# Optimization experiments

Hardware: AMD Instinct MI355X
Metric: run time of the kernel (lower is better)

## Reference

```python
import jax, jax.numpy as jnp
import numpy as np
from jax import lax

# Module constants (from init_kwargs)
K = 1.0            # conductivity
H = 1.0 / 1023.0   # grid spacing
VALUE = 0.0        # Dirichlet boundary value
STENCIL = np.array([[0.0, 0.25, 0.0],
                    [0.25, 0.0, 0.25],
                    [0.0, 0.25, 0.0]], dtype=np.float32)


def setup_inputs() -> dict:
    key = jax.random.key(0)
    k1, k2 = jax.random.split(key)
    B, C, Hn, Wn = 16, 1, 1024, 1024
    u = jax.random.normal(k1, (B, C, Hn, Wn), dtype=jnp.float32)
    f = jax.random.normal(k2, (B, C, Hn, Wn), dtype=jnp.float32)
    # conv weight: (out=1, in=1, 3, 3), repeated over in_channels (=1 here)
    weight = jnp.asarray(STENCIL).reshape(1, 1, 3, 3)
    return {"u": u, "f": f, "weight": weight}


def reference(u, f, weight):
    # v = detached interior of u, padded with the Dirichlet value
    v_int = lax.stop_gradient(u[..., 1:-1, 1:-1])           # [B,1,H-2,W-2]
    v = jnp.pad(v_int, ((0, 0), (0, 0), (1, 1), (1, 1)),
                mode="constant", constant_values=VALUE)      # [B,1,H,W]
    # 5-point Jacobi stencil, VALID conv -> interior shape [B,1,H-2,W-2]
    conv = lax.conv_general_dilated(
        v, weight, window_strides=(1, 1), padding="VALID",
        dimension_numbers=("NCHW", "OIHW", "NCHW"))
    cof = -(H ** 2) / (K * 4.0)
    source = lax.stop_gradient((cof * f)[..., 1:-1, 1:-1])
    # interior <- stencil(v) + source; boundary stays at Dirichlet VALUE
    out = v.at[..., 1:-1, 1:-1].set(conv + source)
    return out
```

## Files before the change

### kernel.cpp

```cpp
#include <hip/hip_runtime.h>

#define IMG_W 1024
#define IMG_H 1024
#define ROWS  8

typedef float v4f __attribute__((ext_vector_type(4)));

__global__ __launch_bounds__(256) void dir_rhs_kernel(
    const float* __restrict__ u,
    const float* __restrict__ f,
    const float* __restrict__ wt,
    float* __restrict__ out)
{
    const int tile = blockIdx.x;
    const int b    = tile >> 7;
    const int r0   = (tile & 127) << 3;
    const int tid  = threadIdx.x;
    const int j0   = tid << 2;
    const size_t img = (size_t)b << 20;

    const float* ub = u   + img;
    const float* fb = f   + img;
    float*       ob = out + img;

    const bool le = (j0 == 0);
    const bool re = (j0 + 4 >= IMG_W);

    const float w00 = wt[0], w01 = wt[1], w02 = wt[2];
    const float w10 = wt[3], w11 = wt[4], w12 = wt[5];
    const float w20 = wt[6], w21 = wt[7], w22 = wt[8];
    const float cof = (float)(-(1.0 / 1023.0) * (1.0 / 1023.0) / 4.0);

    float vm[6], vc[6], vp[6], nx[6];

    auto loadv = [&](float* a, int r) {
        if (r < 1 || r > IMG_H - 2) {
            #pragma unroll
            for (int q = 0; q < 6; q++) a[q] = 0.f;
            return;
        }
        const float* p = ub + (size_t)r * IMG_W;
        v4f c = *(const v4f*)(p + j0);
        a[1] = c.x; a[2] = c.y; a[3] = c.z; a[4] = c.w;
        a[0] = le ? 0.f : p[j0 - 1];
        a[5] = re ? 0.f : p[j0 + 4];
        if (le) a[1] = 0.f;
        if (re) a[4] = 0.f;
    };

    loadv(vm, r0 - 1);
    loadv(vc, r0);
    loadv(vp, r0 + 1);

    #pragma unroll
    for (int k = 0; k < ROWS; k++) {
        const int r = r0 + k;

        loadv(nx, r + 2);

        v4f* o4 = (v4f*)(ob + (size_t)r * IMG_W + j0);

        if (r == 0 || r == IMG_H - 1) {
            v4f z = {0.f, 0.f, 0.f, 0.f};
            __builtin_nontemporal_store(z, o4);
        } else {
            v4f f4 = *(const v4f*)(fb + (size_t)r * IMG_W + j0);
            float ff[4] = {f4.x, f4.y, f4.z, f4.w};

            float res[4];
            #pragma unroll
            for (int e = 0; e < 4; e++) {
                float acc = cof * ff[e];
                acc += w00 * vm[e] + w01 * vm[e + 1] + w02 * vm[e + 2];
                acc += w10 * vc[e] + w11 * vc[e + 1] + w12 * vc[e + 2];
                acc += w20 * vp[e] + w21 * vp[e + 1] + w22 * vp[e + 2];
                res[e] = acc;
            }
            if (le) res[0] = 0.f;
            if (re) res[3] = 0.f;

            v4f rv = {res[0], res[1], res[2], res[3]};
            __builtin_nontemporal_store(rv, o4);
        }

        #pragma unroll
        for (int q = 0; q < 6; q++) { vm[q] = vc[q]; vc[q] = vp[q]; vp[q] = nx[q]; }
    }
}

extern "C" void kernel_launch(void* const* d_in, const int* in_sizes, int n_in,
                              void* d_out, int out_size, void* d_ws, size_t ws_size,
                              hipStream_t stream) {
    const float* u  = (const float*)d_in[0];
    const float* f  = (const float*)d_in[1];
    const float* wt = (const float*)d_in[2];
    float* out = (float*)d_out;

    const int B = 16;
    dim3 grid(B * (IMG_H / ROWS));
    dim3 block(256);
    dir_rhs_kernel<<<grid, block, 0, stream>>>(u, f, wt, out);
}
```

Baseline: 174.4 us.

## Use wavefront shuffles for stencil halos, batch row loads, and swizzle block order

```diff
diff --git a/kernel.cpp b/kernel.cpp
--- a/kernel.cpp
+++ b/kernel.cpp
@@ -2,7 +2,7 @@
 
 #define IMG_W 1024
 #define IMG_H 1024
-#define ROWS  8
+#define ROWS  4
 
 typedef float v4f __attribute__((ext_vector_type(4)));
 
@@ -12,10 +12,13 @@
     const float* __restrict__ wt,
     float* __restrict__ out)
 {
-    const int tile = blockIdx.x;
-    const int b    = tile >> 7;
-    const int r0   = (tile & 127) << 3;
+    const int orig = blockIdx.x;
+    const int tile = (orig & 7) * 512 + (orig >> 3);
+
+    const int b    = tile >> 8;
+    const int r0   = (tile & 255) << 2;
     const int tid  = threadIdx.x;
+    const int lane = tid & 63;
     const int j0   = tid << 2;
     const size_t img = (size_t)b << 20;
 
@@ -24,67 +27,88 @@
     float*       ob = out + img;
 
     const bool le = (j0 == 0);
-    const bool re = (j0 + 4 >= IMG_W);
+    const bool re = (j0 == IMG_W - 4);
 
     const float w00 = wt[0], w01 = wt[1], w02 = wt[2];
     const float w10 = wt[3], w11 = wt[4], w12 = wt[5];
     const float w20 = wt[6], w21 = wt[7], w22 = wt[8];
     const float cof = (float)(-(1.0 / 1023.0) * (1.0 / 1023.0) / 4.0);
 
-    float vm[6], vc[6], vp[6], nx[6];
+    v4f ur[ROWS + 2];
+    #pragma unroll
+    for (int k = 0; k < ROWS + 2; k++) {
+        const int r = r0 - 1 + k;
+        const bool valid = (r >= 1) && (r <= IMG_H - 2);
+        if (valid) {
+            ur[k] = *(const v4f*)(ub + (size_t)r * IMG_W + j0);
+        } else {
+            ur[k] = (v4f){0.f, 0.f, 0.f, 0.f};
+        }
+    }
+    v4f fr[ROWS];
+    #pragma unroll
+    for (int k = 0; k < ROWS; k++) {
+        const int r = r0 + k;
+        if (r >= 1 && r <= IMG_H - 2) {
+            fr[k] = *(const v4f*)(fb + (size_t)r * IMG_W + j0);
+        } else {
+            fr[k] = (v4f){0.f, 0.f, 0.f, 0.f};
+        }
+    }
 
-    auto loadv = [&](float* a, int r) {
-        if (r < 1 || r > IMG_H - 2) {
-            #pragma unroll
-            for (int q = 0; q < 6; q++) a[q] = 0.f;
-            return;
-        }
-        const float* p = ub + (size_t)r * IMG_W;
-        v4f c = *(const v4f*)(p + j0);
-        a[1] = c.x; a[2] = c.y; a[3] = c.z; a[4] = c.w;
-        a[0] = le ? 0.f : p[j0 - 1];
-        a[5] = re ? 0.f : p[j0 + 4];
-        if (le) a[1] = 0.f;
-        if (re) a[4] = 0.f;
-    };
+    float lft[ROWS + 2], rgt[ROWS + 2];
+    #pragma unroll
+    for (int k = 0; k < ROWS + 2; k++) {
+        const int r = r0 - 1 + k;
+        const bool valid = (r >= 1) && (r <= IMG_H - 2);
+        float l  = __shfl_up(ur[k].w, 1);
+        float rr = __shfl_down(ur[k].x, 1);
+        if (valid && lane == 0  && !le) l  = ub[(size_t)r * IMG_W + j0 - 1];
+        if (valid && lane == 63 && !re) rr = ub[(size_t)r * IMG_W + j0 + 4];
+        lft[k] = (le || !valid) ? 0.f : l;
+        rgt[k] = (re || !valid) ? 0.f : rr;
+    }
 
-    loadv(vm, r0 - 1);
-    loadv(vc, r0);
-    loadv(vp, r0 + 1);
+    if (le) {
+        #pragma unroll
+        for (int k = 0; k < ROWS + 2; k++) ur[k].x = 0.f;
+    }
+    if (re) {
+        #pragma unroll
+        for (int k = 0; k < ROWS + 2; k++) ur[k].w = 0.f;
+    }
 
     #pragma unroll
     for (int k = 0; k < ROWS; k++) {
         const int r = r0 + k;
-
-        loadv(nx, r + 2);
-
         v4f* o4 = (v4f*)(ob + (size_t)r * IMG_W + j0);
 
         if (r == 0 || r == IMG_H - 1) {
             v4f z = {0.f, 0.f, 0.f, 0.f};
             __builtin_nontemporal_store(z, o4);
         } else {
-            v4f f4 = *(const v4f*)(fb + (size_t)r * IMG_W + j0);
-            float ff[4] = {f4.x, f4.y, f4.z, f4.w};
-
-            float res[4];
-            #pragma unroll
-            for (int e = 0; e < 4; e++) {
-                float acc = cof * ff[e];
-                acc += w00 * vm[e] + w01 * vm[e + 1] + w02 * vm[e + 2];
-                acc += w10 * vc[e] + w11 * vc[e + 1] + w12 * vc[e + 2];
-                acc += w20 * vp[e] + w21 * vp[e + 1] + w22 * vp[e + 2];
-                res[e] = acc;
-            }
-            if (le) res[0] = 0.f;
-            if (re) res[3] = 0.f;
-
-            v4f rv = {res[0], res[1], res[2], res[3]};
+            const v4f n = ur[k], c = ur[k + 1], s = ur[k + 2];
+            float res0 = cof * fr[k].x
+                       + w00 * lft[k]     + w01 * n.x + w02 * n.y
+                       + w10 * lft[k + 1] + w11 * c.x + w12 * c.y
+                       + w20 * lft[k + 2] + w21 * s.x + w22 * s.y;
+            float res1 = cof * fr[k].y
+                       + w00 * n.x + w01 * n.y + w02 * n.z
+                       + w10 * c.x + w11 * c.y + w12 * c.z
+                       + w20 * s.x + w21 * s.y + w22 * s.z;
+            float res2 = cof * fr[k].z
+                       + w00 * n.y + w01 * n.z + w02 * n.w
+                       + w10 * c.y + w11 * c.z + w12 * c.w
+                       + w20 * s.y + w21 * s.z + w22 * s.w;
+            float res3 = cof * fr[k].w
+                       + w00 * n.z + w01 * n.w + w02 * rgt[k]
+                       + w10 * c.z + w11 * c.w + w12 * rgt[k + 1]
+                       + w20 * s.z + w21 * s.w + w22 * rgt[k + 2];
+            if (le) res0 = 0.f;
+            if (re) res3 = 0.f;
+            v4f rv = {res0, res1, res2, res3};
             __builtin_nontemporal_store(rv, o4);
         }
-
-        #pragma unroll
-        for (int q = 0; q < 6; q++) { vm[q] = vc[q]; vc[q] = vp[q]; vp[q] = nx[q]; }
     }
 }
 
```

After: 180.2 us. +3.3%, slower.

## Process two rows per block with branchless masked loads and XCD-aware tile swizzle

Applied to the files above, without the earlier changes.

```diff
diff --git a/kernel.cpp b/kernel.cpp
--- a/kernel.cpp
+++ b/kernel.cpp
@@ -2,9 +2,9 @@
 
 #define IMG_W 1024
 #define IMG_H 1024
-#define ROWS  8
 
 typedef float v4f __attribute__((ext_vector_type(4)));
+typedef float v2f __attribute__((ext_vector_type(2)));
 
 __global__ __launch_bounds__(256) void dir_rhs_kernel(
     const float* __restrict__ u,
@@ -12,80 +12,86 @@
     const float* __restrict__ wt,
     float* __restrict__ out)
 {
-    const int tile = blockIdx.x;
-    const int b    = tile >> 7;
-    const int r0   = (tile & 127) << 3;
-    const int tid  = threadIdx.x;
-    const int j0   = tid << 2;
+    const int orig = blockIdx.x;
+    const int tile = (orig & 7) * 1024 + (orig >> 3);
+
+    const int b   = tile >> 9;
+    const int i0  = (tile & 511) << 1;
+    const int tid = threadIdx.x;
+    const int j0  = tid << 2;
     const size_t img = (size_t)b << 20;
 
-    const float* ub = u   + img;
-    const float* fb = f   + img;
-    float*       ob = out + img;
+    const float* ub = u + img;
 
     const bool le = (j0 == 0);
-    const bool re = (j0 + 4 >= IMG_W);
+    const bool re = (j0 == IMG_W - 4);
+
+    const int jl = le ? 0         : j0 - 2;
+    const int jr = re ? IMG_W - 2 : j0 + 4;
+
+    v4f c4[4]; v2f lv[4], rv[4]; float m[4];
+    #pragma unroll
+    for (int k = 0; k < 4; k++) {
+        const int li = i0 - 1 + k;
+        const int rc = li < 0 ? 0 : (li > IMG_H - 1 ? IMG_H - 1 : li);
+        const float* p = ub + (size_t)rc * IMG_W;
+        c4[k] = *(const v4f*)(p + j0);
+        lv[k] = *(const v2f*)(p + jl);
+        rv[k] = *(const v2f*)(p + jr);
+        m[k]  = (li >= 1 && li <= IMG_H - 2) ? 1.f : 0.f;
+    }
+    const float* fp = f + img + (size_t)i0 * IMG_W + j0;
+    const v4f f0 = __builtin_nontemporal_load((const v4f*)fp);
+    const v4f f1 = __builtin_nontemporal_load((const v4f*)(fp + IMG_W));
 
     const float w00 = wt[0], w01 = wt[1], w02 = wt[2];
     const float w10 = wt[3], w11 = wt[4], w12 = wt[5];
     const float w20 = wt[6], w21 = wt[7], w22 = wt[8];
     const float cof = (float)(-(1.0 / 1023.0) * (1.0 / 1023.0) / 4.0);
 
-    float vm[6], vc[6], vp[6], nx[6];
+    float lh[4], rh[4];
+    #pragma unroll
+    for (int k = 0; k < 4; k++) {
+        lh[k] = le ? 0.f : lv[k].y * m[k];
+        rh[k] = re ? 0.f : rv[k].x * m[k];
+        c4[k] = c4[k] * m[k];
+        if (le) c4[k].x = 0.f;
+        if (re) c4[k].w = 0.f;
+    }
 
-    auto loadv = [&](float* a, int r) {
-        if (r < 1 || r > IMG_H - 2) {
-            #pragma unroll
-            for (int q = 0; q < 6; q++) a[q] = 0.f;
-            return;
-        }
-        const float* p = ub + (size_t)r * IMG_W;
-        v4f c = *(const v4f*)(p + j0);
-        a[1] = c.x; a[2] = c.y; a[3] = c.z; a[4] = c.w;
-        a[0] = le ? 0.f : p[j0 - 1];
-        a[5] = re ? 0.f : p[j0 + 4];
-        if (le) a[1] = 0.f;
-        if (re) a[4] = 0.f;
+    const float keep0 = (i0 >= 1)         ? 1.f : 0.f;
+    const float keep1 = (i0 <= IMG_H - 3) ? 1.f : 0.f;
+
+    auto stencil = [&](int k, v4f fv, float keep) -> v4f {
+        const v4f n = c4[k], cc = c4[k + 1], s = c4[k + 2];
+        float r0 = cof * fv.x
+                 + w00 * lh[k]     + w01 * n.x  + w02 * n.y
+                 + w10 * lh[k + 1] + w11 * cc.x + w12 * cc.y
+                 + w20 * lh[k + 2] + w21 * s.x  + w22 * s.y;
+        float r1 = cof * fv.y
+                 + w00 * n.x  + w01 * n.y  + w02 * n.z
+                 + w10 * cc.x + w11 * cc.y + w12 * cc.z
+                 + w20 * s.x  + w21 * s.y  + w22 * s.z;
+        float r2 = cof * fv.z
+                 + w00 * n.y  + w01 * n.z  + w02 * n.w
+                 + w10 * cc.y + w11 * cc.z + w12 * cc.w
+                 + w20 * s.y  + w21 * s.z  + w22 * s.w;
+        float r3 = cof * fv.w
+                 + w00 * n.z  + w01 * n.w  + w02 * rh[k]
+                 + w10 * cc.z + w11 * cc.w + w12 * rh[k + 1]
+                 + w20 * s.z  + w21 * s.w  + w22 * rh[k + 2];
+        r0 *= keep; r1 *= keep; r2 *= keep; r3 *= keep;
+        if (le) r0 = 0.f;
+        if (re) r3 = 0.f;
+        return (v4f){r0, r1, r2, r3};
     };
 
-    loadv(vm, r0 - 1);
-    loadv(vc, r0);
-    loadv(vp, r0 + 1);
+    const v4f o0 = stencil(0, f0, keep0);
+    const v4f o1 = stencil(1, f1, keep1);
 
-    #pragma unroll
-    for (int k = 0; k < ROWS; k++) {
-        const int r = r0 + k;
-
-        loadv(nx, r + 2);
-
-        v4f* o4 = (v4f*)(ob + (size_t)r * IMG_W + j0);
-
-        if (r == 0 || r == IMG_H - 1) {
-            v4f z = {0.f, 0.f, 0.f, 0.f};
-            __builtin_nontemporal_store(z, o4);
-        } else {
-            v4f f4 = *(const v4f*)(fb + (size_t)r * IMG_W + j0);
-            float ff[4] = {f4.x, f4.y, f4.z, f4.w};
-
-            float res[4];
-            #pragma unroll
-            for (int e = 0; e < 4; e++) {
-                float acc = cof * ff[e];
-                acc += w00 * vm[e] + w01 * vm[e + 1] + w02 * vm[e + 2];
-                acc += w10 * vc[e] + w11 * vc[e + 1] + w12 * vc[e + 2];
-                acc += w20 * vp[e] + w21 * vp[e + 1] + w22 * vp[e + 2];
-                res[e] = acc;
-            }
-            if (le) res[0] = 0.f;
-            if (re) res[3] = 0.f;
-
-            v4f rv = {res[0], res[1], res[2], res[3]};
-            __builtin_nontemporal_store(rv, o4);
-        }
-
-        #pragma unroll
-        for (int q = 0; q < 6; q++) { vm[q] = vc[q]; vc[q] = vp[q]; vp[q] = nx[q]; }
-    }
+    float* ob = out + img + (size_t)i0 * IMG_W + j0;
+    __builtin_nontemporal_store(o0, (v4f*)ob);
+    __builtin_nontemporal_store(o1, (v4f*)(ob + IMG_W));
 }
 
 extern "C" void kernel_launch(void* const* d_in, const int* in_sizes, int n_in,
@@ -97,7 +103,7 @@
     float* out = (float*)d_out;
 
     const int B = 16;
-    dim3 grid(B * (IMG_H / ROWS));
+    dim3 grid(B * (IMG_H / 2));
     dim3 block(256);
     dir_rhs_kernel<<<grid, block, 0, stream>>>(u, f, wt, out);
 }
```

Result: faster. 168.7 us (-3.3%).
